# Kernel tuning notes

Measured on AMD Instinct MI355X. Metric: run time of the kernel, lower is better.

The kernel has to match this reference:

```python
import jax, jax.numpy as jnp
import numpy as np

HIDDEN = 2048
N_HEADS = 16
HEAD_DIM = HIDDEN // N_HEADS          # 128
KV_CHANNELS = 512
N_KV_HEADS = HIDDEN // KV_CHANNELS    # 4
ROTARY_BASE = 10000.0
ROTARY_DIM = HEAD_DIM                 # rotary_pct = 1.0
SCALE = HEAD_DIM ** -0.5
NEG = -1e9


def setup_inputs() -> dict:
    key = jax.random.key(0)
    k1, k2, k3 = jax.random.split(key, 3)
    B, S = 1, 2048
    hidden_states = jax.random.normal(k1, (B, S, HIDDEN), dtype=jnp.float32)
    # additive causal mask [B,1,S,S]
    causal = jnp.tril(jnp.ones((S, S), dtype=jnp.bool_))
    attention_mask = jnp.where(causal, 0.0, NEG).astype(jnp.float32)[None, None]
    position_ids = jnp.arange(S, dtype=jnp.int64 if jax.config.jax_enable_x64 else jnp.int32)[None].repeat(B, axis=0)
    # torch nn.Linear(in,out) stored as [in,out] so y = x @ W (no bias: no_bias=True)
    qkv_out = N_HEADS * HEAD_DIM + 2 * N_KV_HEADS * HEAD_DIM  # 3072
    W_attn = jax.random.normal(k2, (HIDDEN, qkv_out), dtype=jnp.float32) * (HIDDEN ** -0.5)
    W_proj = jax.random.normal(k3, (HIDDEN, HIDDEN), dtype=jnp.float32) * (HIDDEN ** -0.5)
    return {"hidden_states": hidden_states, "attention_mask": attention_mask,
            "position_ids": position_ids, "W_attn": W_attn, "W_proj": W_proj}


def _rotate_half(x):
    x1, x2 = jnp.split(x, 2, axis=-1)
    return jnp.concatenate([-x2, x1], axis=-1)


def _rope(q, k, position_ids):
    # Faithful to the source: emb = cat(sin(freqs), cos(freqs)); then use cos(emb), sin(emb)
    inv_freq = 1.0 / (ROTARY_BASE ** (jnp.arange(0, ROTARY_DIM, 2, dtype=jnp.float32) / ROTARY_DIM))
    t = position_ids.astype(jnp.float32)                      # [B,S]
    freqs = t[..., None] * inv_freq[None, None, :]            # [B,S,rd/2]
    emb = jnp.concatenate([jnp.sin(freqs), jnp.cos(freqs)], axis=-1)  # [B,S,rd]
    cos_e = jnp.cos(emb)[:, None, :, :]                       # [B,1,S,rd]
    sin_e = jnp.sin(emb)[:, None, :, :]
    q = q * cos_e + _rotate_half(q) * sin_e
    k = k * cos_e + _rotate_half(k) * sin_e
    return q, k


def reference(hidden_states, attention_mask, position_ids, W_attn, W_proj):
    B, S, _ = hidden_states.shape
    qkv = hidden_states @ W_attn                              # [B,S,3072]
    q_len = N_HEADS * HEAD_DIM
    kv_len = N_KV_HEADS * HEAD_DIM
    q, k, v = jnp.split(qkv, [q_len, q_len + kv_len], axis=-1)
    q = q.reshape(B, S, N_HEADS, HEAD_DIM).transpose(0, 2, 1, 3)      # [B,H,S,D]
    k = k.reshape(B, S, N_KV_HEADS, HEAD_DIM).transpose(0, 2, 1, 3)   # [B,Hkv,S,D]
    v = v.reshape(B, S, N_KV_HEADS, HEAD_DIM).transpose(0, 2, 1, 3)
    q, k = _rope(q, k, position_ids)
    # GQA: repeat_interleave over head dim
    rep = N_HEADS // N_KV_HEADS
    k = jnp.repeat(k, rep, axis=1)                            # [B,H,S,D]
    v = jnp.repeat(v, rep, axis=1)
    scores = jnp.einsum('bhqd,bhkd->bhqk', q, k) * SCALE + attention_mask
    probs = jax.nn.softmax(scores, axis=-1)
    attn = jnp.einsum('bhqk,bhkd->bhqd', probs, v)            # [B,H,S,D]
    attn = attn.transpose(0, 2, 1, 3).reshape(B, S, HIDDEN)
    return attn @ W_proj
```

## Files before the change

kernel.cpp:

```cpp
#include <hip/hip_runtime.h>


typedef short s16x8 __attribute__((ext_vector_type(8)));
typedef short s16x4 __attribute__((ext_vector_type(4)));
typedef float f32x4 __attribute__((ext_vector_type(4)));

#define MFMA16 __builtin_amdgcn_mfma_f32_16x16x32_bf16

static constexpr int S = 2048;
static constexpr int HID = 2048;
static constexpr int NH = 16;
static constexpr int HD = 128;
static constexpr int NKV = 4;
static constexpr int QKVN = 3072;
static constexpr float QSCALE = 0.12751743f;

__device__ __forceinline__ short f2bf(float f) {
  unsigned u = __float_as_uint(f);
  unsigned r = (u + 0x7FFFu + ((u >> 16) & 1u)) >> 16;
  return (short)r;
}
__device__ __forceinline__ float bf2f(short s) {
  return __uint_as_float(((unsigned)(unsigned short)s) << 16);
}
__device__ __forceinline__ void gload_lds16(const void* g, void* l) {
  __builtin_amdgcn_global_load_lds(
      (const __attribute__((address_space(1))) unsigned int*)g,
      (__attribute__((address_space(3))) unsigned int*)l, 16, 0, 0);
}

__global__ __launch_bounds__(256) void prep_kernel(
    const float* __restrict__ hidden, const float* __restrict__ Wa,
    const float* __restrict__ Wp, short* __restrict__ hid_bf,
    short* __restrict__ wat, short* __restrict__ wpt) {
  int b = blockIdx.x;
  if (b < 4096) {
    int i = (b * 256 + threadIdx.x) * 4;
    float4 v = *(const float4*)(hidden + i);
    s16x4 o;
    o[0] = f2bf(v.x); o[1] = f2bf(v.y); o[2] = f2bf(v.z); o[3] = f2bf(v.w);
    *(s16x4*)(hid_bf + i) = o;
    return;
  }
  __shared__ float tile[64][33];
  const float* W; short* Wt; int C, bx, by;
  if (b < 7168) {
    W = Wa; Wt = wat; C = QKVN;
    int u = b - 4096; bx = u % 96; by = u / 96;
  } else {
    W = Wp; Wt = wpt; C = HID;
    int u = b - 7168; bx = u & 63; by = u >> 6;
  }
  int c0 = bx * 32, r0 = by * 64;
  int tx = threadIdx.x & 31, ty = threadIdx.x >> 5;
#pragma unroll
  for (int j = 0; j < 8; j++)
    tile[ty + j * 8][tx] = W[(size_t)(r0 + ty + j * 8) * C + c0 + tx];
  __syncthreads();
  int tz = threadIdx.x & 63, tw = threadIdx.x >> 6;
#pragma unroll
  for (int j = 0; j < 8; j++)
    Wt[(size_t)(c0 + tw * 8 + j) * HID + r0 + tz] = f2bf(tile[tz][tw * 8 + j]);
}

__global__ __launch_bounds__(256) void ropevt_kernel(
    const short* __restrict__ qkv, short* __restrict__ Qb,
    short* __restrict__ Kb, short* __restrict__ Vt) {
  int b = blockIdx.x;
  if (b < 2048) {
    int s = b;
    float p = (float)s;
    const short* row = qkv + (size_t)s * QKVN;
#pragma unroll
    for (int j = 0; j < 5; j++) {
      int w = j * 256 + threadIdx.x;
      int hh = w >> 6, i = w & 63;
      float fr = p * __powf(10000.0f, -(float)i / 64.0f);
      float e1 = sinf(fr), e2 = cosf(fr);
      float c1 = cosf(e1), s1 = sinf(e1);
      float c2 = cosf(e2), s2 = sinf(e2);
      if (hh < NH) {
        const short* q = row + hh * HD;
        float a = bf2f(q[i]), bb = bf2f(q[i + 64]);
        Qb[((size_t)hh * S + s) * HD + i] = f2bf((a * c1 - bb * s1) * QSCALE);
        Qb[((size_t)hh * S + s) * HD + i + 64] =
            f2bf((bb * c2 + a * s2) * QSCALE);
      } else {
        int hk = hh - NH;
        const short* k = row + HID + hk * HD;
        float a = bf2f(k[i]), bb = bf2f(k[i + 64]);
        Kb[((size_t)hk * S + s) * HD + i] = f2bf(a * c1 - bb * s1);
        Kb[((size_t)hk * S + s) * HD + i + 64] = f2bf(bb * c2 + a * s2);
      }
    }
    return;
  }
  __shared__ short tile[32][34];
  int u = b - 2048;
  int s0 = (u & 63) * 32, d0 = ((u >> 6) & 3) * 32, hk = u >> 8;
  int tx = threadIdx.x & 31, ty = threadIdx.x >> 5;
#pragma unroll
  for (int j = 0; j < 4; j++)
    tile[ty + j * 8][tx] =
        qkv[(size_t)(s0 + ty + j * 8) * QKVN + 2560 + hk * 128 + d0 + tx];
  __syncthreads();
#pragma unroll
  for (int j = 0; j < 4; j++)
    Vt[((size_t)hk * HD + d0 + ty + j * 8) * S + s0 + tx] = tile[tx][ty + j * 8];
}

template <bool BF16OUT>
__global__ __launch_bounds__(256) void gemm_bt_kernel(
    const short* __restrict__ A, const short* __restrict__ Bt,
    void* __restrict__ Cout, int M, int N, int K) {
  __shared__ short As[3][4096];
  __shared__ short Bs[3][2048];
  int tid = threadIdx.x;
  int lane = tid & 63, wid = tid >> 6;
  int wr = wid >> 1, wc = wid & 1;
  int bm = blockIdx.y * 128, bn = blockIdx.x * 64;
  int srow = tid >> 2;
  int scol = (tid & 3) * 8;
  int rr = lane & 15;
  int kk = (lane >> 4) * 8;

  const short* Ag = A + (size_t)(bm + srow) * K + scol;
  const short* Bg = Bt + (size_t)(bn + srow) * K + scol;
  int ldst = wid * 512;

  f32x4 acc[4][2] = {};

  gload_lds16(Ag, &As[0][ldst]);
  gload_lds16(Ag + (size_t)64 * K, &As[0][ldst + 2048]);
  gload_lds16(Bg, &Bs[0][ldst]);
  Ag += 32; Bg += 32;
  gload_lds16(Ag, &As[1][ldst]);
  gload_lds16(Ag + (size_t)64 * K, &As[1][ldst + 2048]);
  gload_lds16(Bg, &Bs[1][ldst]);
  Ag += 32; Bg += 32;
  asm volatile("s_waitcnt vmcnt(3)" ::: "memory");
  __builtin_amdgcn_sched_barrier(0);
  __builtin_amdgcn_s_barrier();

  int nk = K >> 5;
  int bcur = 0, bpre = 2;
  for (int i = 0; i < nk; ++i) {
    if (i + 2 < nk) {
      gload_lds16(Ag, &As[bpre][ldst]);
      gload_lds16(Ag + (size_t)64 * K, &As[bpre][ldst + 2048]);
      gload_lds16(Bg, &Bs[bpre][ldst]);
      Ag += 32; Bg += 32;
    }
    s16x8 af[4], bfr[2];
#pragma unroll
    for (int m = 0; m < 4; m++)
      af[m] = *(const s16x8*)&As[bcur][(wr * 64 + m * 16 + rr) * 32 + kk];
#pragma unroll
    for (int n = 0; n < 2; n++)
      bfr[n] = *(const s16x8*)&Bs[bcur][(wc * 32 + n * 16 + rr) * 32 + kk];
    __builtin_amdgcn_s_setprio(1);
#pragma unroll
    for (int m = 0; m < 4; m++)
#pragma unroll
      for (int n = 0; n < 2; n++)
        acc[m][n] = MFMA16(af[m], bfr[n], acc[m][n], 0, 0, 0);
    __builtin_amdgcn_s_setprio(0);
    if (i + 2 < nk)
      asm volatile("s_waitcnt vmcnt(3)" ::: "memory");
    else
      asm volatile("s_waitcnt vmcnt(0)" ::: "memory");
    __builtin_amdgcn_sched_barrier(0);
    __builtin_amdgcn_s_barrier();
    __builtin_amdgcn_sched_barrier(0);
    bcur = (bcur == 2) ? 0 : bcur + 1;
    bpre = (bpre == 2) ? 0 : bpre + 1;
  }

  int crow0 = bm + wr * 64 + (lane >> 4) * 4;
  int ccol0 = bn + wc * 32 + rr;
#pragma unroll
  for (int m = 0; m < 4; m++)
#pragma unroll
    for (int n = 0; n < 2; n++)
#pragma unroll
      for (int r = 0; r < 4; r++) {
        size_t idx = (size_t)(crow0 + m * 16 + r) * N + ccol0 + n * 16;
        if (BF16OUT) ((short*)Cout)[idx] = f2bf(acc[m][n][r]);
        else ((float*)Cout)[idx] = acc[m][n][r];
      }
}

__global__ __launch_bounds__(256) void attn_kernel(
    const short* __restrict__ Q, const short* __restrict__ K,
    const short* __restrict__ Vt, short* __restrict__ Ob) {
  __shared__ short Ks[2][8192];
  __shared__ short Vs[2][8192];
  __shared__ short Pl[4][16][72];
  int wid = threadIdx.x >> 6, lane = threadIdx.x & 63;
  int gid = blockIdx.x;
  int g = gid & 255;
  int h = g & 15;
  int v = (g >> 4) & 15;
  int qb = (gid < 256) ? 31 - v : v;
  int hk = h >> 2;
  int q0 = qb * 64 + wid * 16;
  int rr = lane & 15, rg = lane >> 4, r7 = rr & 7;

  const short* Qh = Q + ((size_t)h * S + q0) * HD;
  s16x8 qf[4];
#pragma unroll
  for (int kc = 0; kc < 4; kc++)
    qf[kc] = *(const s16x8*)(Qh + rr * HD + kc * 32 + rg * 8);

  const short* Kh = K + (size_t)hk * S * HD;
  const short* Vh = Vt + (size_t)hk * HD * S;

  size_t koff[4], voff[4];
  int kdst[4], vdst[4];
#pragma unroll
  for (int g2 = 0; g2 < 4; g2++) {
    int kr = wid * 16 + g2 * 4 + (lane >> 4);
    koff[g2] = (size_t)kr * 128 + 8 * ((lane & 15) ^ (kr & 7));
    kdst[g2] = (wid * 16 + g2 * 4) * 128;
    int vr = wid * 32 + g2 * 8 + (lane >> 3);
    voff[g2] = (size_t)vr * S + 8 * ((lane & 7) ^ (vr & 7));
    vdst[g2] = (wid * 32 + g2 * 8) * 64;
  }

  f32x4 o[8] = {};
  float mrow[4], plr[4];
#pragma unroll
  for (int r = 0; r < 4; r++) { mrow[r] = -1e30f; plr[r] = 0.0f; }

#pragma unroll
  for (int g2 = 0; g2 < 4; g2++) {
    gload_lds16(Kh + koff[g2], &Ks[0][kdst[g2]]);
    gload_lds16(Vh + voff[g2], &Vs[0][vdst[g2]]);
  }
  asm volatile("s_waitcnt vmcnt(0)" ::: "memory");
  __syncthreads();

  for (int t = 0; t <= qb; ++t) {
    int buf = t & 1;
    if (t < qb) {
      size_t kvs = (size_t)(t + 1) * 64;
#pragma unroll
      for (int g2 = 0; g2 < 4; g2++) {
        gload_lds16(Kh + kvs * 128 + koff[g2], &Ks[buf ^ 1][kdst[g2]]);
        gload_lds16(Vh + kvs + voff[g2], &Vs[buf ^ 1][vdst[g2]]);
      }
    }
    int kvb = t * 64;
    const short* Kb_ = Ks[buf];
    const short* Vb_ = Vs[buf];

    f32x4 sc4[4];
    __builtin_amdgcn_s_setprio(1);
#pragma unroll
    for (int c = 0; c < 4; c++) {
      f32x4 sacc = {};
#pragma unroll
      for (int kc = 0; kc < 4; kc++) {
        int chunk = (rg + kc * 4) ^ r7;
        s16x8 kf = *(const s16x8*)(Kb_ + (c * 16 + rr) * 128 + chunk * 8);
        sacc = MFMA16(qf[kc], kf, sacc, 0, 0, 0);
      }
      sc4[c] = sacc;
    }
    __builtin_amdgcn_s_setprio(0);

#pragma unroll
    for (int r = 0; r < 4; r++) {
      float v0 = sc4[0][r], v1 = sc4[1][r];
      float v2 = sc4[2][r], v3 = sc4[3][r];
      if (t == qb) {
        int qrow = q0 + rg * 4 + r;
        v0 += (kvb + rr) > qrow ? -1e9f : 0.0f;
        v1 += (kvb + 16 + rr) > qrow ? -1e9f : 0.0f;
        v2 += (kvb + 32 + rr) > qrow ? -1e9f : 0.0f;
        v3 += (kvb + 48 + rr) > qrow ? -1e9f : 0.0f;
      }
      float pmax = fmaxf(fmaxf(v0, v1), fmaxf(v2, v3));
      unsigned long long bal = __ballot(pmax > mrow[r] + 11.5f);
      if ((bal >> (rg * 16)) & 0xFFFFull) {
        float mx = pmax;
#pragma unroll
        for (int d = 1; d < 16; d <<= 1) mx = fmaxf(mx, __shfl_xor(mx, d, 64));
        float mn = fmaxf(mrow[r], mx);
        float scl = exp2f(mrow[r] - mn);
        mrow[r] = mn;
        plr[r] *= scl;
#pragma unroll
        for (int dc = 0; dc < 8; dc++) o[dc][r] *= scl;
      }
      float p0 = exp2f(v0 - mrow[r]), p1 = exp2f(v1 - mrow[r]);
      float p2 = exp2f(v2 - mrow[r]), p3 = exp2f(v3 - mrow[r]);
      plr[r] += (p0 + p1) + (p2 + p3);
      Pl[wid][rg * 4 + r][rr] = f2bf(p0);
      Pl[wid][rg * 4 + r][rr + 16] = f2bf(p1);
      Pl[wid][rg * 4 + r][rr + 32] = f2bf(p2);
      Pl[wid][rg * 4 + r][rr + 48] = f2bf(p3);
    }
    asm volatile("s_waitcnt lgkmcnt(0)" ::: "memory");
    __builtin_amdgcn_sched_barrier(0);
    s16x8 pf0 = *(const s16x8*)&Pl[wid][rr][rg * 8];
    s16x8 pf1 = *(const s16x8*)&Pl[wid][rr][32 + rg * 8];

    __builtin_amdgcn_s_setprio(1);
#pragma unroll
    for (int dc = 0; dc < 8; dc++) {
      int ch0 = rg ^ r7, ch1 = (rg + 4) ^ r7;
      s16x8 vf0 = *(const s16x8*)(Vb_ + (dc * 16 + rr) * 64 + ch0 * 8);
      s16x8 vf1 = *(const s16x8*)(Vb_ + (dc * 16 + rr) * 64 + ch1 * 8);
      o[dc] = MFMA16(pf0, vf0, o[dc], 0, 0, 0);
      o[dc] = MFMA16(pf1, vf1, o[dc], 0, 0, 0);
    }
    __builtin_amdgcn_s_setprio(0);

    asm volatile("s_waitcnt vmcnt(0)" ::: "memory");
    __syncthreads();
  }

#pragma unroll
  for (int r = 0; r < 4; r++) {
    float l = plr[r];
#pragma unroll
    for (int d = 1; d < 16; d <<= 1) l += __shfl_xor(l, d, 64);
    float inv = 1.0f / l;
    int srow = q0 + rg * 4 + r;
#pragma unroll
    for (int dc = 0; dc < 8; dc++)
      Ob[(size_t)srow * HID + h * HD + dc * 16 + rr] = f2bf(o[dc][r] * inv);
  }
}

extern "C" void kernel_launch(void* const* d_in, const int* in_sizes, int n_in,
                              void* d_out, int out_size, void* d_ws,
                              size_t ws_size, hipStream_t stream) {
  (void)in_sizes; (void)n_in; (void)out_size; (void)ws_size;
  const float* hidden = (const float*)d_in[0];
  const float* W_attn = (const float*)d_in[3];
  const float* W_proj = (const float*)d_in[4];
  float* out = (float*)d_out;

  char* ws = (char*)d_ws;
  short* hid_bf = (short*)(ws);
  short* wat    = (short*)(ws + 8388608);
  short* wpt    = (short*)(ws + 20971520);
  short* qkvb   = (short*)(ws + 29360128);
  short* Qb     = (short*)(ws + 41943040);
  short* Kb     = (short*)(ws + 50331648);
  short* Vt     = (short*)(ws + 52428800);
  short* Ab     = (short*)(ws + 54525952);

  hipLaunchKernelGGL(prep_kernel, dim3(9216), dim3(256), 0, stream,
                     hidden, W_attn, W_proj, hid_bf, wat, wpt);
  hipLaunchKernelGGL((gemm_bt_kernel<true>), dim3(QKVN / 64, S / 128),
                     dim3(256), 0, stream, hid_bf, wat, (void*)qkvb, S, QKVN,
                     HID);
  hipLaunchKernelGGL(ropevt_kernel, dim3(3072), dim3(256), 0, stream,
                     qkvb, Qb, Kb, Vt);
  hipLaunchKernelGGL(attn_kernel, dim3(512), dim3(256), 0, stream,
                     Qb, Kb, Vt, Ab);
  hipLaunchKernelGGL((gemm_bt_kernel<false>), dim3(HID / 64, S / 128),
                     dim3(256), 0, stream, Ab, wpt, (void*)out, S, HID, HID);
}
```

Measured before the change: 273.9 us.

## Deepen GEMM LDS pipeline to four stages and remap blocks per XCD

The GEMM kernel now keeps four shared-memory buffers with three tiles in flight instead of three buffers with two. Wait counts are adjusted for the deeper prefetch, and the barrier is skipped after the final iteration. Block indices are also remapped so each of the 8 XCDs handles a contiguous range of N-tiles, which should improve L2 reuse of the B operand. The cost is more LDS per block, which may lower occupancy, and a mapping that assumes the N-tile count divides by 8.

```diff
diff --git a/kernel.cpp b/kernel.cpp
--- a/kernel.cpp
+++ b/kernel.cpp
@@ -112,13 +112,17 @@
 template <bool BF16OUT>
 __global__ __launch_bounds__(256) void gemm_bt_kernel(
     const short* __restrict__ A, const short* __restrict__ Bt,
-    void* __restrict__ Cout, int M, int N, int K) {
-  __shared__ short As[3][4096];
-  __shared__ short Bs[3][2048];
+    void* __restrict__ Cout, int M, int N, int K, int nbn) {
+  __shared__ short As[4][4096];
+  __shared__ short Bs[4][2048];
   int tid = threadIdx.x;
   int lane = tid & 63, wid = tid >> 6;
   int wr = wid >> 1, wc = wid & 1;
-  int bm = blockIdx.y * 128, bn = blockIdx.x * 64;
+  int bid = blockIdx.y * gridDim.x + blockIdx.x;
+  int cbn = nbn >> 3;
+  int xcd = bid & 7, slot = bid >> 3;
+  int bm = (slot / cbn) * 128;
+  int bn = (xcd * cbn + slot % cbn) * 64;
   int srow = tid >> 2;
   int scol = (tid & 3) * 8;
   int rr = lane & 15;
@@ -130,22 +134,22 @@
 
   f32x4 acc[4][2] = {};
 
-  gload_lds16(Ag, &As[0][ldst]);
-  gload_lds16(Ag + (size_t)64 * K, &As[0][ldst + 2048]);
-  gload_lds16(Bg, &Bs[0][ldst]);
-  Ag += 32; Bg += 32;
-  gload_lds16(Ag, &As[1][ldst]);
-  gload_lds16(Ag + (size_t)64 * K, &As[1][ldst + 2048]);
-  gload_lds16(Bg, &Bs[1][ldst]);
-  Ag += 32; Bg += 32;
-  asm volatile("s_waitcnt vmcnt(3)" ::: "memory");
+#pragma unroll
+  for (int d = 0; d < 3; ++d) {
+    gload_lds16(Ag, &As[d][ldst]);
+    gload_lds16(Ag + (size_t)64 * K, &As[d][ldst + 2048]);
+    gload_lds16(Bg, &Bs[d][ldst]);
+    Ag += 32; Bg += 32;
+  }
+  asm volatile("s_waitcnt vmcnt(6)" ::: "memory");
   __builtin_amdgcn_sched_barrier(0);
   __builtin_amdgcn_s_barrier();
 
   int nk = K >> 5;
-  int bcur = 0, bpre = 2;
   for (int i = 0; i < nk; ++i) {
-    if (i + 2 < nk) {
+    int bcur = i & 3;
+    if (i + 3 < nk) {
+      int bpre = (i + 3) & 3;
       gload_lds16(Ag, &As[bpre][ldst]);
       gload_lds16(Ag + (size_t)64 * K, &As[bpre][ldst + 2048]);
       gload_lds16(Bg, &Bs[bpre][ldst]);
@@ -165,15 +169,17 @@
       for (int n = 0; n < 2; n++)
         acc[m][n] = MFMA16(af[m], bfr[n], acc[m][n], 0, 0, 0);
     __builtin_amdgcn_s_setprio(0);
-    if (i + 2 < nk)
-      asm volatile("s_waitcnt vmcnt(3)" ::: "memory");
-    else
-      asm volatile("s_waitcnt vmcnt(0)" ::: "memory");
-    __builtin_amdgcn_sched_barrier(0);
-    __builtin_amdgcn_s_barrier();
-    __builtin_amdgcn_sched_barrier(0);
-    bcur = (bcur == 2) ? 0 : bcur + 1;
-    bpre = (bpre == 2) ? 0 : bpre + 1;
+    if (i + 1 < nk) {
+      if (i + 3 < nk)
+        asm volatile("s_waitcnt vmcnt(6)" ::: "memory");
+      else if (i + 2 < nk)
+        asm volatile("s_waitcnt vmcnt(3)" ::: "memory");
+      else
+        asm volatile("s_waitcnt vmcnt(0)" ::: "memory");
+      __builtin_amdgcn_sched_barrier(0);
+      __builtin_amdgcn_s_barrier();
+      __builtin_amdgcn_sched_barrier(0);
+    }
   }
 
   int crow0 = bm + wr * 64 + (lane >> 4) * 4;
@@ -357,11 +363,12 @@
                      hidden, W_attn, W_proj, hid_bf, wat, wpt);
   hipLaunchKernelGGL((gemm_bt_kernel<true>), dim3(QKVN / 64, S / 128),
                      dim3(256), 0, stream, hid_bf, wat, (void*)qkvb, S, QKVN,
-                     HID);
+                     HID, QKVN / 64);
   hipLaunchKernelGGL(ropevt_kernel, dim3(3072), dim3(256), 0, stream,
                      qkvb, Qb, Kb, Vt);
   hipLaunchKernelGGL(attn_kernel, dim3(512), dim3(256), 0, stream,
                      Qb, Kb, Vt, Ab);
   hipLaunchKernelGGL((gemm_bt_kernel<false>), dim3(HID / 64, S / 128),
-                     dim3(256), 0, stream, Ab, wpt, (void*)out, S, HID, HID);
-}
+                     dim3(256), 0, stream, Ab, wpt, (void*)out, S, HID, HID,
+                     HID / 64);
+}
```

Measured after the change: 271.4 us. About the same (-0.9%).
